# Performance work log

Measured on AMD Instinct MI355X. Metric: run time of the kernel, lower is better.

## Reference

```python
import jax, jax.numpy as jnp
import numpy as np

N_NODES = 50000
N_EDGES = 640000
N_FEAT = 512
HIDDEN = 128
N_CLASSES = 64


def setup_inputs() -> dict:
    key = jax.random.key(0)
    k1, k2, k3, k4, k5, k6 = jax.random.split(key, 6)
    x = jax.random.normal(k1, (N_NODES, N_FEAT), dtype=jnp.float32)
    edge_index = jax.random.randint(k2, (2, N_EDGES), 0, N_NODES, dtype=jnp.int32)
    # GCNConv weights (glorot-ish scale) and biases
    W1 = jax.random.normal(k3, (N_FEAT, HIDDEN), dtype=jnp.float32) / np.sqrt(N_FEAT)
    b1 = jnp.zeros((HIDDEN,), dtype=jnp.float32)
    W2 = jax.random.normal(k4, (HIDDEN, N_CLASSES), dtype=jnp.float32) / np.sqrt(HIDDEN)
    b2 = jnp.zeros((N_CLASSES,), dtype=jnp.float32)
    return {"x": x, "edge_index": edge_index, "W1": W1, "b1": b1, "W2": W2, "b2": b2}


def reference(x, edge_index, W1, b1, W2, b2):
    N = x.shape[0]
    # Add self-loops (PyG GCNConv default)
    loop = jnp.arange(N, dtype=edge_index.dtype)
    src = jnp.concatenate([edge_index[0], loop])
    dst = jnp.concatenate([edge_index[1], loop])
    # Symmetric normalization: deg computed over targets incl. self-loops
    deg = jax.ops.segment_sum(jnp.ones(src.shape[0], dtype=x.dtype), dst, num_segments=N)
    dinv = jax.lax.rsqrt(deg)  # deg >= 1 thanks to self-loops
    norm = dinv[src] * dinv[dst]  # [E+N]

    def gcn_conv(h, W, b):
        h = h @ W                          # dense transform first (smaller msg dim)
        msg = h[src] * norm[:, None]       # gather + normalize
        return jax.ops.segment_sum(msg, dst, num_segments=N) + b  # scatter-add + bias

    h = jax.nn.relu(gcn_conv(x, W1, b1))
    # F.dropout with training=False is identity (eval mode)
    return gcn_conv(h, W2, b2)
```

## Files before the change

kernel.cpp:

```cpp
#include <hip/hip_runtime.h>


#define NNODES 50000
#define NEDGES 640000
#define NFEAT 512
#define NHID 128
#define NCLS 64

typedef _Float16 f16x8 __attribute__((ext_vector_type(8)));
typedef _Float16 f16x2 __attribute__((ext_vector_type(2)));
typedef float f32x4 __attribute__((ext_vector_type(4)));

__device__ __forceinline__ void g2l16(const void* g, void* s) {
  __builtin_amdgcn_global_load_lds(
      (const __attribute__((address_space(1))) void*)g,
      (__attribute__((address_space(3))) void*)s, 16, 0, 0);
}

__global__ void k_zero2(int* __restrict__ a, int* __restrict__ b, int n) {
  int i = blockIdx.x * blockDim.x + threadIdx.x;
  if (i < n) { a[i] = 0; b[i] = 0; }
}

__global__ void k_hist(const int* __restrict__ dst, int* __restrict__ indeg, int E) {
  int i = blockIdx.x * blockDim.x + threadIdx.x;
  if (i < E) atomicAdd(&indeg[dst[i]], 1);
}

__global__ void k_scan_block(const int* __restrict__ indeg, float* __restrict__ dinv,
                             int* __restrict__ row_start, int* __restrict__ blocksum,
                             int n) {
  __shared__ int sdata[256];
  int t = threadIdx.x;
  int base = blockIdx.x * 1024 + t * 4;
  int v[4];
#pragma unroll
  for (int j = 0; j < 4; ++j) {
    int idx = base + j;
    int d = (idx < n) ? indeg[idx] : 0;
    if (idx < n) dinv[idx] = 1.0f / sqrtf((float)(d + 1));
    v[j] = (d + 3) & ~3;
  }
  int tsum = v[0] + v[1] + v[2] + v[3];
  sdata[t] = tsum;
  __syncthreads();
  for (int off = 1; off < 256; off <<= 1) {
    int x = (t >= off) ? sdata[t - off] : 0;
    __syncthreads();
    sdata[t] += x;
    __syncthreads();
  }
  int excl = sdata[t] - tsum;
  if (t == 255) blocksum[blockIdx.x] = sdata[255];
  int run = excl;
#pragma unroll
  for (int j = 0; j < 4; ++j) {
    if (base + j <= n) { row_start[base + j] = run; run += v[j]; }
  }
}

__global__ void k_scan_top(const int* __restrict__ blocksum, int* __restrict__ blockoff, int nb) {
  if (threadIdx.x == 0 && blockIdx.x == 0) {
    int run = 0;
    for (int i = 0; i < nb; ++i) { blockoff[i] = run; run += blocksum[i]; }
  }
}

__global__ void k_scan_add(int* __restrict__ row_start, const int* __restrict__ blockoff,
                           const int* __restrict__ indeg, int* __restrict__ csr_src,
                           float* __restrict__ csr_norm, int n) {
  int i = blockIdx.x * blockDim.x + threadIdx.x;
  if (i <= n) {
    int rs = row_start[i] + blockoff[i >> 10];
    row_start[i] = rs;
    if (i < n) {
      int d = indeg[i];
      int p = (d + 3) & ~3;
      for (int j = d; j < p; ++j) { csr_src[rs + j] = i; csr_norm[rs + j] = 0.f; }
    }
  }
}

__global__ void k_scatter(const int* __restrict__ src, const int* __restrict__ dst,
                          const int* __restrict__ row_start, int* __restrict__ cursor,
                          const float* __restrict__ dinv, int* __restrict__ csr_src,
                          float* __restrict__ csr_norm, int E) {
  int e = blockIdx.x * blockDim.x + threadIdx.x;
  if (e < E) {
    int s = src[e], d = dst[e];
    int pos = atomicAdd(&cursor[d], 1);
    int idx = row_start[d] + pos;
    csr_src[idx] = s;
    csr_norm[idx] = dinv[s] * dinv[d];
  }
}

__global__ void k_wcvt(const float* __restrict__ W, _Float16* __restrict__ Wt_hi,
                       _Float16* __restrict__ Wt_lo, int K, int Nc) {
  int i = blockIdx.x * blockDim.x + threadIdx.x;
  if (i < K * Nc) {
    int k = i / Nc, n = i % Nc;
    float v = W[i];
    _Float16 h = (_Float16)v;
    Wt_hi[(size_t)n * K + k] = h;
    Wt_lo[(size_t)n * K + k] = (_Float16)((v - (float)h) * 1024.0f);
  }
}

__global__ __launch_bounds__(256) void k_gemm1(const float* __restrict__ A,
                                               const _Float16* __restrict__ Bhi,
                                               const _Float16* __restrict__ Blo,
                                               float* __restrict__ C, int M) {
  __shared__ char smem[49152];
  constexpr int A_OFF = 0;
  constexpr int BH_OFF = 16384;
  constexpr int BL_OFF = 32768;
  const int tid = threadIdx.x;
  const int wid = tid >> 6, lane = tid & 63;
  const int wy = wid >> 1, wx = wid & 1;
  const int row0 = blockIdx.x * 64;
  const int lrow = lane & 15;
  const int lkg = lane >> 4;

  auto stage = [&](int buf, int k0) {
#pragma unroll
    for (int c = 0; c < 2; ++c) {
      int idx = c * 256 + tid;
      int row = idx >> 3;
      int kq = (idx & 7) ^ (row & 7);
      int gr = row0 + row; gr = gr < M ? gr : M - 1;
      g2l16((const char*)A + (size_t)gr * 2048 + (size_t)k0 * 4 + kq * 16,
            smem + A_OFF + buf * 8192 + ((idx & ~63) << 4));
    }
#pragma unroll
    for (int c = 0; c < 2; ++c) {
      int idx = c * 256 + tid;
      int n = idx >> 2;
      int kq = (idx & 3) ^ (n & 3);
      size_t so = (size_t)n * 1024 + (size_t)k0 * 2 + kq * 16;
      g2l16((const char*)Bhi + so, smem + BH_OFF + buf * 8192 + ((idx & ~63) << 4));
      g2l16((const char*)Blo + so, smem + BL_OFF + buf * 8192 + ((idx & ~63) << 4));
    }
  };

  f32x4 acc_h[2][4] = {};
  f32x4 acc_l[2][4] = {};

  stage(0, 0);
  __syncthreads();
  int cur = 0;
  constexpr int NK = NFEAT / 32;
  for (int ks = 0; ks < NK; ++ks) {
    if (ks + 1 < NK) stage(cur ^ 1, (ks + 1) * 32);

    const char* ab = smem + A_OFF + cur * 8192;
    const char* bhb = smem + BH_OFF + cur * 8192;
    const char* blb = smem + BL_OFF + cur * 8192;
    f16x8 ah[2], al[2], bh[4], bl[4];
#pragma unroll
    for (int rf = 0; rf < 2; ++rf) {
      int r = wy * 32 + rf * 16 + lrow;
      int lin = r * 128 + lkg * 32;
      int sw = (r & 7) << 4;
      float4 v0 = *(const float4*)(ab + (lin ^ sw));
      float4 v1 = *(const float4*)(ab + ((lin + 16) ^ sw));
      float vv[8] = {v0.x, v0.y, v0.z, v0.w, v1.x, v1.y, v1.z, v1.w};
#pragma unroll
      for (int j = 0; j < 8; ++j) {
        _Float16 h = (_Float16)vv[j];
        ah[rf][j] = h;
        al[rf][j] = (_Float16)((vv[j] - (float)h) * 1024.0f);
      }
    }
#pragma unroll
    for (int cf = 0; cf < 4; ++cf) {
      int n = wx * 64 + cf * 16 + lrow;
      int lin = n * 64 + lkg * 16;
      int sw = (n & 3) << 4;
      bh[cf] = *(const f16x8*)(bhb + (lin ^ sw));
      bl[cf] = *(const f16x8*)(blb + (lin ^ sw));
    }
#pragma unroll
    for (int rf = 0; rf < 2; ++rf)
#pragma unroll
      for (int cf = 0; cf < 4; ++cf) {
        acc_h[rf][cf] = __builtin_amdgcn_mfma_f32_16x16x32_f16(ah[rf], bh[cf],
                                                               acc_h[rf][cf], 0, 0, 0);
        acc_l[rf][cf] = __builtin_amdgcn_mfma_f32_16x16x32_f16(ah[rf], bl[cf],
                                                               acc_l[rf][cf], 0, 0, 0);
        acc_l[rf][cf] = __builtin_amdgcn_mfma_f32_16x16x32_f16(al[rf], bh[cf],
                                                               acc_l[rf][cf], 0, 0, 0);
      }
    if (ks + 1 < NK) { __syncthreads(); cur ^= 1; }
  }

#pragma unroll
  for (int rf = 0; rf < 2; ++rf) {
    int rfrag = row0 + wy * 32 + rf * 16;
    if (rfrag >= M) continue;
    int rbase = rfrag + lkg * 4;
#pragma unroll
    for (int cf = 0; cf < 4; ++cf) {
      int col = wx * 64 + cf * 16 + lrow;
#pragma unroll
      for (int q = 0; q < 4; ++q)
        C[(size_t)(rbase + q) * NHID + col] =
            acc_h[rf][cf][q] + acc_l[rf][cf][q] * (1.0f / 1024.0f);
    }
  }
}

__global__ __launch_bounds__(256) void k_gemm2(const _Float16* __restrict__ Ahi,
                                               const _Float16* __restrict__ Alo,
                                               const _Float16* __restrict__ Bhi,
                                               const _Float16* __restrict__ Blo,
                                               float* __restrict__ C, int M) {
  __shared__ char smem[32768];
  constexpr int AH_OFF = 0;
  constexpr int AL_OFF = 8192;
  constexpr int BH_OFF = 16384;
  constexpr int BL_OFF = 24576;
  const int tid = threadIdx.x;
  const int wid = tid >> 6, lane = tid & 63;
  const int row0 = blockIdx.x * 64;
  const int lrow = lane & 15;
  const int lkg = lane >> 4;

  auto stage = [&](int buf, int k0) {
    int idx = tid;
    int row = idx >> 2;
    int kq = (idx & 3) ^ (row & 3);
    int gr = row0 + row; gr = gr < M ? gr : M - 1;
    size_t aso = (size_t)gr * 256 + (size_t)k0 * 2 + kq * 16;
    size_t bso = (size_t)row * 256 + (size_t)k0 * 2 + kq * 16;
    int ldso = (idx & ~63) << 4;
    g2l16((const char*)Ahi + aso, smem + AH_OFF + buf * 4096 + ldso);
    g2l16((const char*)Alo + aso, smem + AL_OFF + buf * 4096 + ldso);
    g2l16((const char*)Bhi + bso, smem + BH_OFF + buf * 4096 + ldso);
    g2l16((const char*)Blo + bso, smem + BL_OFF + buf * 4096 + ldso);
  };

  f32x4 acc_h[4] = {};
  f32x4 acc_l[4] = {};

  stage(0, 0);
  __syncthreads();
  int cur = 0;
  constexpr int NK = NHID / 32;
  for (int ks = 0; ks < NK; ++ks) {
    if (ks + 1 < NK) stage(cur ^ 1, (ks + 1) * 32);

    const char* ahb = smem + AH_OFF + cur * 4096;
    const char* alb = smem + AL_OFF + cur * 4096;
    const char* bhb = smem + BH_OFF + cur * 4096;
    const char* blb = smem + BL_OFF + cur * 4096;
    int r = wid * 16 + lrow;
    int alin = r * 64 + lkg * 16;
    int asw = (r & 3) << 4;
    f16x8 ah = *(const f16x8*)(ahb + (alin ^ asw));
    f16x8 al = *(const f16x8*)(alb + (alin ^ asw));
    f16x8 bh[4], bl[4];
#pragma unroll
    for (int cf = 0; cf < 4; ++cf) {
      int n = cf * 16 + lrow;
      int lin = n * 64 + lkg * 16;
      int sw = (n & 3) << 4;
      bh[cf] = *(const f16x8*)(bhb + (lin ^ sw));
      bl[cf] = *(const f16x8*)(blb + (lin ^ sw));
    }
#pragma unroll
    for (int cf = 0; cf < 4; ++cf) {
      acc_h[cf] = __builtin_amdgcn_mfma_f32_16x16x32_f16(ah, bh[cf], acc_h[cf], 0, 0, 0);
      acc_l[cf] = __builtin_amdgcn_mfma_f32_16x16x32_f16(ah, bl[cf], acc_l[cf], 0, 0, 0);
      acc_l[cf] = __builtin_amdgcn_mfma_f32_16x16x32_f16(al, bh[cf], acc_l[cf], 0, 0, 0);
    }
    if (ks + 1 < NK) { __syncthreads(); cur ^= 1; }
  }

  int rfrag = row0 + wid * 16;
  if (rfrag < M) {
    int rbase = rfrag + lkg * 4;
#pragma unroll
    for (int cf = 0; cf < 4; ++cf) {
      int col = cf * 16 + lrow;
#pragma unroll
      for (int q = 0; q < 4; ++q)
        C[(size_t)(rbase + q) * NCLS + col] =
            acc_h[cf][q] + acc_l[cf][q] * (1.0f / 1024.0f);
    }
  }
}

template <bool RELU, bool EMIT16>
__global__ __launch_bounds__(256) void k_agg128(
    const float* __restrict__ h, const float* __restrict__ bias,
    const int* __restrict__ row_start, const int* __restrict__ csr_src,
    const float* __restrict__ csr_norm, const float* __restrict__ dinv,
    float* __restrict__ out, _Float16* __restrict__ out_hi,
    _Float16* __restrict__ out_lo, int N) {
  int node = blockIdx.x * 4 + (threadIdx.x >> 6);
  if (node >= N) return;
  int lane = threadIdx.x & 63;
  const float2* hp = (const float2*)h;

  float dn = dinv[node];
  float2 bs = ((const float2*)bias)[lane];
  float2 sf = hp[(size_t)node * 64 + lane];
  float2 a0 = {dn * dn * sf.x + bs.x, dn * dn * sf.y + bs.y};
  float2 a1 = {0.f, 0.f}, a2 = {0.f, 0.f}, a3 = {0.f, 0.f};
  float2 a4 = {0.f, 0.f}, a5 = {0.f, 0.f}, a6 = {0.f, 0.f}, a7 = {0.f, 0.f};

  int e = row_start[node], e1 = row_start[node + 1];
#define GATH(ACC, EI)                                        \
  {                                                          \
    int s_ = csr_src[EI];                                    \
    float w_ = csr_norm[EI];                                 \
    float2 v_ = hp[(size_t)s_ * 64 + lane];                  \
    ACC.x += w_ * v_.x;                                      \
    ACC.y += w_ * v_.y;                                      \
  }
  for (; e + 8 <= e1; e += 8) {
    GATH(a0, e + 0) GATH(a1, e + 1) GATH(a2, e + 2) GATH(a3, e + 3)
    GATH(a4, e + 4) GATH(a5, e + 5) GATH(a6, e + 6) GATH(a7, e + 7)
  }
  if (e < e1) {
    GATH(a0, e + 0) GATH(a1, e + 1) GATH(a2, e + 2) GATH(a3, e + 3)
  }
#undef GATH
  float ax = ((a0.x + a1.x) + (a2.x + a3.x)) + ((a4.x + a5.x) + (a6.x + a7.x));
  float ay = ((a0.y + a1.y) + (a2.y + a3.y)) + ((a4.y + a5.y) + (a6.y + a7.y));
  if (RELU) { ax = fmaxf(ax, 0.f); ay = fmaxf(ay, 0.f); }
  if (EMIT16) {
    _Float16 hx = (_Float16)ax, hy = (_Float16)ay;
    f16x2 vh = {hx, hy};
    f16x2 vl = {(_Float16)((ax - (float)hx) * 1024.0f),
                (_Float16)((ay - (float)hy) * 1024.0f)};
    *(f16x2*)(out_hi + (size_t)node * 128 + lane * 2) = vh;
    *(f16x2*)(out_lo + (size_t)node * 128 + lane * 2) = vl;
  } else {
    ((float2*)out)[(size_t)node * 64 + lane] = {ax, ay};
  }
}

__global__ __launch_bounds__(256) void k_agg64(
    const float* __restrict__ h, const float* __restrict__ bias,
    const int* __restrict__ row_start, const int* __restrict__ csr_src,
    const float* __restrict__ csr_norm, const float* __restrict__ dinv,
    float* __restrict__ out, int N) {
  int node = blockIdx.x * 4 + (threadIdx.x >> 6);
  if (node >= N) return;
  int f = threadIdx.x & 63;
  float dn = dinv[node];
  float a0 = dn * dn * h[(size_t)node * 64 + f] + bias[f];
  float a1 = 0.f, a2 = 0.f, a3 = 0.f, a4 = 0.f, a5 = 0.f, a6 = 0.f, a7 = 0.f;
  int e = row_start[node], e1 = row_start[node + 1];
#define GATH(ACC, EI) ACC += csr_norm[EI] * h[(size_t)csr_src[EI] * 64 + f];
  for (; e + 8 <= e1; e += 8) {
    GATH(a0, e + 0) GATH(a1, e + 1) GATH(a2, e + 2) GATH(a3, e + 3)
    GATH(a4, e + 4) GATH(a5, e + 5) GATH(a6, e + 6) GATH(a7, e + 7)
  }
  if (e < e1) {
    GATH(a0, e + 0) GATH(a1, e + 1) GATH(a2, e + 2) GATH(a3, e + 3)
  }
#undef GATH
  out[(size_t)node * 64 + f] =
      ((a0 + a1) + (a2 + a3)) + ((a4 + a5) + (a6 + a7));
}

static inline size_t align256(size_t x) { return (x + 255) & ~(size_t)255; }

extern "C" void kernel_launch(void* const* d_in, const int* in_sizes, int n_in,
                              void* d_out, int out_size, void* d_ws, size_t ws_size,
                              hipStream_t stream) {
  const float* x = (const float*)d_in[0];
  const int* edge = (const int*)d_in[1];
  const float* W1 = (const float*)d_in[2];
  const float* b1 = (const float*)d_in[3];
  const float* W2 = (const float*)d_in[4];
  const float* b2 = (const float*)d_in[5];
  float* out = (float*)d_out;

  const int N = NNODES;
  const int E = NEDGES;
  const int EPAD = E + 3 * N + 256;
  const int* src = edge;
  const int* dst = edge + E;

  char* w = (char*)d_ws;
  int* indeg = (int*)w;            w += align256((size_t)N * 4);
  int* cursor = (int*)w;           w += align256((size_t)N * 4);
  float* dinv = (float*)w;         w += align256((size_t)N * 4);
  int* row_start = (int*)w;        w += align256((size_t)(N + 1) * 4);
  int* blocksum = (int*)w;         w += align256(64 * 4);
  int* blockoff = (int*)w;         w += align256(64 * 4);
  int* csr_src = (int*)w;          w += align256((size_t)EPAD * 4);
  float* csr_norm = (float*)w;     w += align256((size_t)EPAD * 4);
  _Float16* W1t_hi = (_Float16*)w; w += align256((size_t)NFEAT * NHID * 2);
  _Float16* W1t_lo = (_Float16*)w; w += align256((size_t)NFEAT * NHID * 2);
  _Float16* W2t_hi = (_Float16*)w; w += align256((size_t)NHID * NCLS * 2);
  _Float16* W2t_lo = (_Float16*)w; w += align256((size_t)NHID * NCLS * 2);
  float* h0 = (float*)w;           w += align256((size_t)N * NHID * 4);
  _Float16* h1_hi = (_Float16*)w;  w += align256((size_t)N * NHID * 2);
  _Float16* h1_lo = (_Float16*)w;  w += align256((size_t)N * NHID * 2);
  float* h2 = (float*)w;           w += align256((size_t)N * NCLS * 4);

  const int nblk_n = (N + 255) / 256;
  const int nblk_n1 = (N + 1 + 255) / 256;
  const int nblk_e = (E + 255) / 256;
  const int nblk_scan = (N + 1 + 1023) / 1024;

  k_zero2<<<nblk_n, 256, 0, stream>>>(indeg, cursor, N);
  k_hist<<<nblk_e, 256, 0, stream>>>(dst, indeg, E);
  k_scan_block<<<nblk_scan, 256, 0, stream>>>(indeg, dinv, row_start, blocksum, N);
  k_scan_top<<<1, 64, 0, stream>>>(blocksum, blockoff, nblk_scan);
  k_scan_add<<<nblk_n1, 256, 0, stream>>>(row_start, blockoff, indeg, csr_src,
                                          csr_norm, N);
  k_scatter<<<nblk_e, 256, 0, stream>>>(src, dst, row_start, cursor, dinv,
                                        csr_src, csr_norm, E);

  k_wcvt<<<(NFEAT * NHID + 255) / 256, 256, 0, stream>>>(W1, W1t_hi, W1t_lo,
                                                         NFEAT, NHID);
  k_wcvt<<<(NHID * NCLS + 255) / 256, 256, 0, stream>>>(W2, W2t_hi, W2t_lo,
                                                        NHID, NCLS);

  k_gemm1<<<(N + 63) / 64, 256, 0, stream>>>(x, W1t_hi, W1t_lo, h0, N);
  k_agg128<true, true><<<(N + 3) / 4, 256, 0, stream>>>(
      h0, b1, row_start, csr_src, csr_norm, dinv, nullptr, h1_hi, h1_lo, N);
  k_gemm2<<<(N + 63) / 64, 256, 0, stream>>>(h1_hi, h1_lo, W2t_hi, W2t_lo, h2, N);
  k_agg64<<<(N + 3) / 4, 256, 0, stream>>>(h2, b2, row_start, csr_src, csr_norm,
                                           dinv, out, N);
}
```

Before: 350.8 us.

## Pack CSR as int2, widen aggregation loads, retile gemm1 to 512 threads

Merges the CSR source index and edge weight into one int2 array so each edge needs one 8-byte load instead of two. The aggregation kernels now have each lane gather 4 floats, so one wavefront covers 2 or 4 nodes and fewer wave-wide index loads are issued. gemm1 moves to 512 threads with one row fragment per wave, which cuts accumulator registers per thread but gives less reuse of each B fragment. The LDS swizzle in both GEMMs gains an extra XOR term to reduce bank conflicts.

```diff
diff --git a/kernel.cpp b/kernel.cpp
--- a/kernel.cpp
+++ b/kernel.cpp
@@ -8,7 +8,7 @@
 #define NCLS 64
 
 typedef _Float16 f16x8 __attribute__((ext_vector_type(8)));
-typedef _Float16 f16x2 __attribute__((ext_vector_type(2)));
+typedef _Float16 f16x4 __attribute__((ext_vector_type(4)));
 typedef float f32x4 __attribute__((ext_vector_type(4)));
 
 __device__ __forceinline__ void g2l16(const void* g, void* s) {
@@ -67,8 +67,8 @@
 }
 
 __global__ void k_scan_add(int* __restrict__ row_start, const int* __restrict__ blockoff,
-                           const int* __restrict__ indeg, int* __restrict__ csr_src,
-                           float* __restrict__ csr_norm, int n) {
+                           const int* __restrict__ indeg, int2* __restrict__ csr,
+                           int n) {
   int i = blockIdx.x * blockDim.x + threadIdx.x;
   if (i <= n) {
     int rs = row_start[i] + blockoff[i >> 10];
@@ -76,22 +76,20 @@
     if (i < n) {
       int d = indeg[i];
       int p = (d + 3) & ~3;
-      for (int j = d; j < p; ++j) { csr_src[rs + j] = i; csr_norm[rs + j] = 0.f; }
+      for (int j = d; j < p; ++j) csr[rs + j] = make_int2(i, 0);
     }
   }
 }
 
 __global__ void k_scatter(const int* __restrict__ src, const int* __restrict__ dst,
                           const int* __restrict__ row_start, int* __restrict__ cursor,
-                          const float* __restrict__ dinv, int* __restrict__ csr_src,
-                          float* __restrict__ csr_norm, int E) {
+                          const float* __restrict__ dinv, int2* __restrict__ csr, int E) {
   int e = blockIdx.x * blockDim.x + threadIdx.x;
   if (e < E) {
     int s = src[e], d = dst[e];
     int pos = atomicAdd(&cursor[d], 1);
-    int idx = row_start[d] + pos;
-    csr_src[idx] = s;
-    csr_norm[idx] = dinv[s] * dinv[d];
+    float w = dinv[s] * dinv[d];
+    csr[row_start[d] + pos] = make_int2(s, __float_as_int(w));
   }
 }
 
@@ -107,10 +105,10 @@
   }
 }
 
-__global__ __launch_bounds__(256) void k_gemm1(const float* __restrict__ A,
-                                               const _Float16* __restrict__ Bhi,
-                                               const _Float16* __restrict__ Blo,
-                                               float* __restrict__ C, int M) {
+__global__ __launch_bounds__(512, 6) void k_gemm1(const float* __restrict__ A,
+                                                  const _Float16* __restrict__ Bhi,
+                                                  const _Float16* __restrict__ Blo,
+                                                  float* __restrict__ C, int M) {
   __shared__ char smem[49152];
   constexpr int A_OFF = 0;
   constexpr int BH_OFF = 16384;
@@ -123,28 +121,24 @@
   const int lkg = lane >> 4;
 
   auto stage = [&](int buf, int k0) {
-#pragma unroll
-    for (int c = 0; c < 2; ++c) {
-      int idx = c * 256 + tid;
-      int row = idx >> 3;
-      int kq = (idx & 7) ^ (row & 7);
+    {
+      int row = tid >> 3;
+      int kq = (tid & 7) ^ (row & 7);
       int gr = row0 + row; gr = gr < M ? gr : M - 1;
       g2l16((const char*)A + (size_t)gr * 2048 + (size_t)k0 * 4 + kq * 16,
-            smem + A_OFF + buf * 8192 + ((idx & ~63) << 4));
-    }
-#pragma unroll
-    for (int c = 0; c < 2; ++c) {
-      int idx = c * 256 + tid;
-      int n = idx >> 2;
-      int kq = (idx & 3) ^ (n & 3);
+            smem + A_OFF + buf * 8192 + ((tid & ~63) << 4));
+    }
+    {
+      int n = tid >> 2;
+      int kq = (tid & 3) ^ (n & 3) ^ ((n >> 2) & 3);
       size_t so = (size_t)n * 1024 + (size_t)k0 * 2 + kq * 16;
-      g2l16((const char*)Bhi + so, smem + BH_OFF + buf * 8192 + ((idx & ~63) << 4));
-      g2l16((const char*)Blo + so, smem + BL_OFF + buf * 8192 + ((idx & ~63) << 4));
+      g2l16((const char*)Bhi + so, smem + BH_OFF + buf * 8192 + ((tid & ~63) << 4));
+      g2l16((const char*)Blo + so, smem + BL_OFF + buf * 8192 + ((tid & ~63) << 4));
     }
   };
 
-  f32x4 acc_h[2][4] = {};
-  f32x4 acc_l[2][4] = {};
+  f32x4 acc_h[4] = {};
+  f32x4 acc_l[4] = {};
 
   stage(0, 0);
   __syncthreads();
@@ -156,10 +150,9 @@
     const char* ab = smem + A_OFF + cur * 8192;
     const char* bhb = smem + BH_OFF + cur * 8192;
     const char* blb = smem + BL_OFF + cur * 8192;
-    f16x8 ah[2], al[2], bh[4], bl[4];
-#pragma unroll
-    for (int rf = 0; rf < 2; ++rf) {
-      int r = wy * 32 + rf * 16 + lrow;
+    f16x8 ah, al, bh[4], bl[4];
+    {
+      int r = wy * 16 + lrow;
       int lin = r * 128 + lkg * 32;
       int sw = (r & 7) << 4;
       float4 v0 = *(const float4*)(ab + (lin ^ sw));
@@ -168,36 +161,29 @@
 #pragma unroll
       for (int j = 0; j < 8; ++j) {
         _Float16 h = (_Float16)vv[j];
-        ah[rf][j] = h;
-        al[rf][j] = (_Float16)((vv[j] - (float)h) * 1024.0f);
+        ah[j] = h;
+        al[j] = (_Float16)((vv[j] - (float)h) * 1024.0f);
       }
     }
 #pragma unroll
     for (int cf = 0; cf < 4; ++cf) {
       int n = wx * 64 + cf * 16 + lrow;
-      int lin = n * 64 + lkg * 16;
-      int sw = (n & 3) << 4;
-      bh[cf] = *(const f16x8*)(bhb + (lin ^ sw));
-      bl[cf] = *(const f16x8*)(blb + (lin ^ sw));
-    }
-#pragma unroll
-    for (int rf = 0; rf < 2; ++rf)
-#pragma unroll
-      for (int cf = 0; cf < 4; ++cf) {
-        acc_h[rf][cf] = __builtin_amdgcn_mfma_f32_16x16x32_f16(ah[rf], bh[cf],
-                                                               acc_h[rf][cf], 0, 0, 0);
-        acc_l[rf][cf] = __builtin_amdgcn_mfma_f32_16x16x32_f16(ah[rf], bl[cf],
-                                                               acc_l[rf][cf], 0, 0, 0);
-        acc_l[rf][cf] = __builtin_amdgcn_mfma_f32_16x16x32_f16(al[rf], bh[cf],
-                                                               acc_l[rf][cf], 0, 0, 0);
-      }
+      int slot = lkg ^ (n & 3) ^ ((n >> 2) & 3);
+      int lin = n * 64 + slot * 16;
+      bh[cf] = *(const f16x8*)(bhb + lin);
+      bl[cf] = *(const f16x8*)(blb + lin);
+    }
+#pragma unroll
+    for (int cf = 0; cf < 4; ++cf) {
+      acc_h[cf] = __builtin_amdgcn_mfma_f32_16x16x32_f16(ah, bh[cf], acc_h[cf], 0, 0, 0);
+      acc_l[cf] = __builtin_amdgcn_mfma_f32_16x16x32_f16(ah, bl[cf], acc_l[cf], 0, 0, 0);
+      acc_l[cf] = __builtin_amdgcn_mfma_f32_16x16x32_f16(al, bh[cf], acc_l[cf], 0, 0, 0);
+    }
     if (ks + 1 < NK) { __syncthreads(); cur ^= 1; }
   }
 
-#pragma unroll
-  for (int rf = 0; rf < 2; ++rf) {
-    int rfrag = row0 + wy * 32 + rf * 16;
-    if (rfrag >= M) continue;
+  int rfrag = row0 + wy * 16;
+  if (rfrag < M) {
     int rbase = rfrag + lkg * 4;
 #pragma unroll
     for (int cf = 0; cf < 4; ++cf) {
@@ -205,7 +191,7 @@
 #pragma unroll
       for (int q = 0; q < 4; ++q)
         C[(size_t)(rbase + q) * NHID + col] =
-            acc_h[rf][cf][q] + acc_l[rf][cf][q] * (1.0f / 1024.0f);
+            acc_h[cf][q] + acc_l[cf][q] * (1.0f / 1024.0f);
     }
   }
 }
@@ -227,13 +213,12 @@
   const int lkg = lane >> 4;
 
   auto stage = [&](int buf, int k0) {
-    int idx = tid;
-    int row = idx >> 2;
-    int kq = (idx & 3) ^ (row & 3);
+    int row = tid >> 2;
+    int kq = (tid & 3) ^ (row & 3) ^ ((row >> 2) & 3);
     int gr = row0 + row; gr = gr < M ? gr : M - 1;
     size_t aso = (size_t)gr * 256 + (size_t)k0 * 2 + kq * 16;
     size_t bso = (size_t)row * 256 + (size_t)k0 * 2 + kq * 16;
-    int ldso = (idx & ~63) << 4;
+    int ldso = (tid & ~63) << 4;
     g2l16((const char*)Ahi + aso, smem + AH_OFF + buf * 4096 + ldso);
     g2l16((const char*)Alo + aso, smem + AL_OFF + buf * 4096 + ldso);
     g2l16((const char*)Bhi + bso, smem + BH_OFF + buf * 4096 + ldso);
@@ -255,18 +240,18 @@
     const char* bhb = smem + BH_OFF + cur * 4096;
     const char* blb = smem + BL_OFF + cur * 4096;
     int r = wid * 16 + lrow;
-    int alin = r * 64 + lkg * 16;
-    int asw = (r & 3) << 4;
-    f16x8 ah = *(const f16x8*)(ahb + (alin ^ asw));
-    f16x8 al = *(const f16x8*)(alb + (alin ^ asw));
+    int aslot = lkg ^ (r & 3) ^ ((r >> 2) & 3);
+    int alin = r * 64 + aslot * 16;
+    f16x8 ah = *(const f16x8*)(ahb + alin);
+    f16x8 al = *(const f16x8*)(alb + alin);
     f16x8 bh[4], bl[4];
 #pragma unroll
     for (int cf = 0; cf < 4; ++cf) {
       int n = cf * 16 + lrow;
-      int lin = n * 64 + lkg * 16;
-      int sw = (n & 3) << 4;
-      bh[cf] = *(const f16x8*)(bhb + (lin ^ sw));
-      bl[cf] = *(const f16x8*)(blb + (lin ^ sw));
+      int slot = lkg ^ (n & 3) ^ ((n >> 2) & 3);
+      int lin = n * 64 + slot * 16;
+      bh[cf] = *(const f16x8*)(bhb + lin);
+      bl[cf] = *(const f16x8*)(blb + lin);
     }
 #pragma unroll
     for (int cf = 0; cf < 4; ++cf) {
@@ -294,30 +279,28 @@
 template <bool RELU, bool EMIT16>
 __global__ __launch_bounds__(256) void k_agg128(
     const float* __restrict__ h, const float* __restrict__ bias,
-    const int* __restrict__ row_start, const int* __restrict__ csr_src,
-    const float* __restrict__ csr_norm, const float* __restrict__ dinv,
-    float* __restrict__ out, _Float16* __restrict__ out_hi,
-    _Float16* __restrict__ out_lo, int N) {
-  int node = blockIdx.x * 4 + (threadIdx.x >> 6);
+    const int* __restrict__ row_start, const int2* __restrict__ csr,
+    const float* __restrict__ dinv, float* __restrict__ out,
+    _Float16* __restrict__ out_hi, _Float16* __restrict__ out_lo, int N) {
+  int tid = threadIdx.x;
+  int lane = tid & 63;
+  int node = blockIdx.x * 8 + (tid >> 6) * 2 + (lane >> 5);
   if (node >= N) return;
-  int lane = threadIdx.x & 63;
-  const float2* hp = (const float2*)h;
+  int li = lane & 31;
 
   float dn = dinv[node];
-  float2 bs = ((const float2*)bias)[lane];
-  float2 sf = hp[(size_t)node * 64 + lane];
-  float2 a0 = {dn * dn * sf.x + bs.x, dn * dn * sf.y + bs.y};
-  float2 a1 = {0.f, 0.f}, a2 = {0.f, 0.f}, a3 = {0.f, 0.f};
-  float2 a4 = {0.f, 0.f}, a5 = {0.f, 0.f}, a6 = {0.f, 0.f}, a7 = {0.f, 0.f};
+  f32x4 bs = *(const f32x4*)(bias + li * 4);
+  f32x4 sf = *(const f32x4*)(h + (size_t)node * 128 + li * 4);
+  f32x4 a0 = dn * dn * sf + bs;
+  f32x4 a1 = {}, a2 = {}, a3 = {}, a4 = {}, a5 = {}, a6 = {}, a7 = {};
 
   int e = row_start[node], e1 = row_start[node + 1];
-#define GATH(ACC, EI)                                        \
-  {                                                          \
-    int s_ = csr_src[EI];                                    \
-    float w_ = csr_norm[EI];                                 \
-    float2 v_ = hp[(size_t)s_ * 64 + lane];                  \
-    ACC.x += w_ * v_.x;                                      \
-    ACC.y += w_ * v_.y;                                      \
+#define GATH(ACC, EI)                                              \
+  {                                                                \
+    int2 p_ = csr[EI];                                             \
+    float w_ = __int_as_float(p_.y);                               \
+    f32x4 v_ = *(const f32x4*)(h + (size_t)p_.x * 128 + li * 4);   \
+    ACC += w_ * v_;                                                \
   }
   for (; e + 8 <= e1; e += 8) {
     GATH(a0, e + 0) GATH(a1, e + 1) GATH(a2, e + 2) GATH(a3, e + 3)
@@ -327,34 +310,50 @@
     GATH(a0, e + 0) GATH(a1, e + 1) GATH(a2, e + 2) GATH(a3, e + 3)
   }
 #undef GATH
-  float ax = ((a0.x + a1.x) + (a2.x + a3.x)) + ((a4.x + a5.x) + (a6.x + a7.x));
-  float ay = ((a0.y + a1.y) + (a2.y + a3.y)) + ((a4.y + a5.y) + (a6.y + a7.y));
-  if (RELU) { ax = fmaxf(ax, 0.f); ay = fmaxf(ay, 0.f); }
+  f32x4 acc = ((a0 + a1) + (a2 + a3)) + ((a4 + a5) + (a6 + a7));
+  if (RELU) {
+#pragma unroll
+    for (int j = 0; j < 4; ++j) acc[j] = fmaxf(acc[j], 0.f);
+  }
   if (EMIT16) {
-    _Float16 hx = (_Float16)ax, hy = (_Float16)ay;
-    f16x2 vh = {hx, hy};
-    f16x2 vl = {(_Float16)((ax - (float)hx) * 1024.0f),
-                (_Float16)((ay - (float)hy) * 1024.0f)};
-    *(f16x2*)(out_hi + (size_t)node * 128 + lane * 2) = vh;
-    *(f16x2*)(out_lo + (size_t)node * 128 + lane * 2) = vl;
+    f16x4 vh, vl;
+#pragma unroll
+    for (int j = 0; j < 4; ++j) {
+      _Float16 hh = (_Float16)acc[j];
+      vh[j] = hh;
+      vl[j] = (_Float16)((acc[j] - (float)hh) * 1024.0f);
+    }
+    *(f16x4*)(out_hi + (size_t)node * 128 + li * 4) = vh;
+    *(f16x4*)(out_lo + (size_t)node * 128 + li * 4) = vl;
   } else {
-    ((float2*)out)[(size_t)node * 64 + lane] = {ax, ay};
+    *(f32x4*)(out + (size_t)node * 128 + li * 4) = acc;
   }
 }
 
 __global__ __launch_bounds__(256) void k_agg64(
     const float* __restrict__ h, const float* __restrict__ bias,
-    const int* __restrict__ row_start, const int* __restrict__ csr_src,
-    const float* __restrict__ csr_norm, const float* __restrict__ dinv,
-    float* __restrict__ out, int N) {
-  int node = blockIdx.x * 4 + (threadIdx.x >> 6);
+    const int* __restrict__ row_start, const int2* __restrict__ csr,
+    const float* __restrict__ dinv, float* __restrict__ out, int N) {
+  int tid = threadIdx.x;
+  int lane = tid & 63;
+  int node = blockIdx.x * 16 + (tid >> 6) * 4 + (lane >> 4);
   if (node >= N) return;
-  int f = threadIdx.x & 63;
+  int li = lane & 15;
+
   float dn = dinv[node];
-  float a0 = dn * dn * h[(size_t)node * 64 + f] + bias[f];
-  float a1 = 0.f, a2 = 0.f, a3 = 0.f, a4 = 0.f, a5 = 0.f, a6 = 0.f, a7 = 0.f;
+  f32x4 bs = *(const f32x4*)(bias + li * 4);
+  f32x4 sf = *(const f32x4*)(h + (size_t)node * 64 + li * 4);
+  f32x4 a0 = dn * dn * sf + bs;
+  f32x4 a1 = {}, a2 = {}, a3 = {}, a4 = {}, a5 = {}, a6 = {}, a7 = {};
+
   int e = row_start[node], e1 = row_start[node + 1];
-#define GATH(ACC, EI) ACC += csr_norm[EI] * h[(size_t)csr_src[EI] * 64 + f];
+#define GATH(ACC, EI)                                             \
+  {                                                               \
+    int2 p_ = csr[EI];                                            \
+    float w_ = __int_as_float(p_.y);                              \
+    f32x4 v_ = *(const f32x4*)(h + (size_t)p_.x * 64 + li * 4);   \
+    ACC += w_ * v_;                                               \
+  }
   for (; e + 8 <= e1; e += 8) {
     GATH(a0, e + 0) GATH(a1, e + 1) GATH(a2, e + 2) GATH(a3, e + 3)
     GATH(a4, e + 4) GATH(a5, e + 5) GATH(a6, e + 6) GATH(a7, e + 7)
@@ -363,8 +362,8 @@
     GATH(a0, e + 0) GATH(a1, e + 1) GATH(a2, e + 2) GATH(a3, e + 3)
   }
 #undef GATH
-  out[(size_t)node * 64 + f] =
-      ((a0 + a1) + (a2 + a3)) + ((a4 + a5) + (a6 + a7));
+  f32x4 acc = ((a0 + a1) + (a2 + a3)) + ((a4 + a5) + (a6 + a7));
+  *(f32x4*)(out + (size_t)node * 64 + li * 4) = acc;
 }
 
 static inline size_t align256(size_t x) { return (x + 255) & ~(size_t)255; }
@@ -393,8 +392,7 @@
   int* row_start = (int*)w;        w += align256((size_t)(N + 1) * 4);
   int* blocksum = (int*)w;         w += align256(64 * 4);
   int* blockoff = (int*)w;         w += align256(64 * 4);
-  int* csr_src = (int*)w;          w += align256((size_t)EPAD * 4);
-  float* csr_norm = (float*)w;     w += align256((size_t)EPAD * 4);
+  int2* csr = (int2*)w;            w += align256((size_t)EPAD * 8);
   _Float16* W1t_hi = (_Float16*)w; w += align256((size_t)NFEAT * NHID * 2);
   _Float16* W1t_lo = (_Float16*)w; w += align256((size_t)NFEAT * NHID * 2);
   _Float16* W2t_hi = (_Float16*)w; w += align256((size_t)NHID * NCLS * 2);
@@ -413,20 +411,17 @@
   k_hist<<<nblk_e, 256, 0, stream>>>(dst, indeg, E);
   k_scan_block<<<nblk_scan, 256, 0, stream>>>(indeg, dinv, row_start, blocksum, N);
   k_scan_top<<<1, 64, 0, stream>>>(blocksum, blockoff, nblk_scan);
-  k_scan_add<<<nblk_n1, 256, 0, stream>>>(row_start, blockoff, indeg, csr_src,
-                                          csr_norm, N);
-  k_scatter<<<nblk_e, 256, 0, stream>>>(src, dst, row_start, cursor, dinv,
-                                        csr_src, csr_norm, E);
+  k_scan_add<<<nblk_n1, 256, 0, stream>>>(row_start, blockoff, indeg, csr, N);
+  k_scatter<<<nblk_e, 256, 0, stream>>>(src, dst, row_start, cursor, dinv, csr, E);
 
   k_wcvt<<<(NFEAT * NHID + 255) / 256, 256, 0, stream>>>(W1, W1t_hi, W1t_lo,
                                                          NFEAT, NHID);
   k_wcvt<<<(NHID * NCLS + 255) / 256, 256, 0, stream>>>(W2, W2t_hi, W2t_lo,
                                                         NHID, NCLS);
 
-  k_gemm1<<<(N + 63) / 64, 256, 0, stream>>>(x, W1t_hi, W1t_lo, h0, N);
-  k_agg128<true, true><<<(N + 3) / 4, 256, 0, stream>>>(
-      h0, b1, row_start, csr_src, csr_norm, dinv, nullptr, h1_hi, h1_lo, N);
+  k_gemm1<<<(N + 63) / 64, 512, 0, stream>>>(x, W1t_hi, W1t_lo, h0, N);
+  k_agg128<true, true><<<(N + 7) / 8, 256, 0, stream>>>(
+      h0, b1, row_start, csr, dinv, nullptr, h1_hi, h1_lo, N);
   k_gemm2<<<(N + 63) / 64, 256, 0, stream>>>(h1_hi, h1_lo, W2t_hi, W2t_lo, h2, N);
-  k_agg64<<<(N + 3) / 4, 256, 0, stream>>>(h2, b2, row_start, csr_src, csr_norm,
-                                           dinv, out, N);
-}
+  k_agg64<<<(N + 15) / 16, 256, 0, stream>>>(h2, b2, row_start, csr, dinv, out, N);
+}
```

Result: slower. 358.1 us (+2.1%).
